# Optimization experiments

Hardware: AMD Instinct MI355X
Metric: run time of the kernel (lower is better)

Reference implementation:

```python
import jax, jax.numpy as jnp
import numpy as np

N = 100000   # num nodes
E = 800000   # num edges
D = 16       # latent_dim
K = 3        # message-passing iterations
ALPHA = 0.1
GAMMA = 0.9


def _mlp2(x, w1, b1, w2, b2):
    return jax.nn.relu(x @ w1 + b1) @ w2 + b2


def setup_inputs() -> dict:
    key = jax.random.key(0)
    ks = iter(jax.random.split(key, 40))
    def w(shape, fan_in):
        return jax.random.normal(next(ks), shape, jnp.float32) / np.sqrt(fan_in)
    return {
        "edge_index": jax.random.randint(next(ks), (2, E), 0, N),
        "edge_attr": jax.random.normal(next(ks), (E, 3), jnp.float32),
        "a_ij": jax.random.normal(next(ks), (E, 1), jnp.float32),
        "prb_data": jax.random.normal(next(ks), (N, 1), jnp.float32),
        "sol": jax.random.normal(next(ks), (N, 1), jnp.float32),
        "y": jax.random.normal(next(ks), (N, 1), jnp.float32),
        "phi_to_w1": w((K, 2 * D + 3, D), 2 * D + 3), "phi_to_b1": jnp.zeros((K, D), jnp.float32),
        "phi_to_w2": w((K, D, D), D), "phi_to_b2": jnp.zeros((K, D), jnp.float32),
        "phi_from_w1": w((K, 2 * D + 3, D), 2 * D + 3), "phi_from_b1": jnp.zeros((K, D), jnp.float32),
        "phi_from_w2": w((K, D, D), D), "phi_from_b2": jnp.zeros((K, D), jnp.float32),
        "psi_w1": w((K, 3 * D + 1, D), 3 * D + 1), "psi_b1": jnp.zeros((K, D), jnp.float32),
        "psi_w2": w((K, D, D), D), "psi_b2": jnp.zeros((K, D), jnp.float32),
        "dec_w1": w((K, D, D), D), "dec_b1": jnp.zeros((K, D), jnp.float32),
        "dec_w2": w((K, D, 1), D), "dec_b2": jnp.zeros((K, 1), jnp.float32),
    }


def reference(edge_index, edge_attr, a_ij, prb_data, sol, y,
              phi_to_w1, phi_to_b1, phi_to_w2, phi_to_b2,
              phi_from_w1, phi_from_b1, phi_from_w2, phi_from_b2,
              psi_w1, psi_b1, psi_w2, psi_b2,
              dec_w1, dec_b1, dec_w2, dec_b2):
    src, dst = edge_index[0], edge_index[1]
    # remove_self_loops: with 'add' aggregation, zeroing self-loop messages is equivalent.
    sl_mask = (src != dst).astype(edge_attr.dtype)[:, None]

    def message_pass(h, xi_idx, xj_idx, agg_idx, w1, b1, w2, b2):
        # gather-concat-MLP-scatter: tmp is [E, 2D+3]
        tmp = jnp.concatenate([h[xi_idx], h[xj_idx], edge_attr], axis=1)
        m = _mlp2(tmp, w1, b1, w2, b2) * sl_mask
        return jax.ops.segment_sum(m, agg_idx, num_segments=N)

    a_val = a_ij[:, 0]
    def residual_loss(u):
        # SparseTensor(row=src, col=dst, value=a_ij) @ u  (self-loops kept here)
        Au = jax.ops.segment_sum(a_val * u[dst, 0], src, num_segments=N)[:, None]
        return jnp.mean((Au - y) ** 2)

    h = jnp.zeros((N, D), edge_attr.dtype)
    u = _mlp2(h, dec_w1[0], dec_b1[0], dec_w2[0], dec_b2[0])  # U['0']
    total_loss = jnp.zeros((), edge_attr.dtype)
    for t in range(K):
        # Phi_to: flow source_to_target -> x_i = h[dst], x_j = h[src], aggregate at dst
        mess_to = message_pass(h, dst, src, dst, phi_to_w1[t], phi_to_b1[t], phi_to_w2[t], phi_to_b2[t])
        # Phi_from: flow target_to_source -> x_i = h[src], x_j = h[dst], aggregate at src
        mess_from = message_pass(h, src, dst, src, phi_from_w1[t], phi_from_b1[t], phi_from_w2[t], phi_from_b2[t])
        concat = jnp.concatenate([h, mess_to, mess_from, prb_data], axis=1)  # [N, 3D+1]
        h = h + ALPHA * _mlp2(concat, psi_w1[t], psi_b1[t], psi_w2[t], psi_b2[t])
        u = _mlp2(h, dec_w1[t], dec_b1[t], dec_w2[t], dec_b2[t])
        total_loss = total_loss + residual_loss(u) * GAMMA ** (K - t - 1)
    return u, total_loss
```

## Files before the change

kernel.cpp:

```cpp
#include <hip/hip_runtime.h>

#define NN 100000
#define NE 800000
#define DD 16
#define ALPHA 0.1f

__device__ __forceinline__ void load16(const float* __restrict__ p, float* r) {
  float4 v0 = *(const float4*)(p + 0);
  float4 v1 = *(const float4*)(p + 4);
  float4 v2 = *(const float4*)(p + 8);
  float4 v3 = *(const float4*)(p + 12);
  r[0]=v0.x; r[1]=v0.y; r[2]=v0.z; r[3]=v0.w;
  r[4]=v1.x; r[5]=v1.y; r[6]=v1.z; r[7]=v1.w;
  r[8]=v2.x; r[9]=v2.y; r[10]=v2.z; r[11]=v2.w;
  r[12]=v3.x; r[13]=v3.y; r[14]=v3.z; r[15]=v3.w;
}

__device__ __forceinline__ void store16(float* __restrict__ p, const float* r) {
  *(float4*)(p + 0)  = make_float4(r[0], r[1], r[2], r[3]);
  *(float4*)(p + 4)  = make_float4(r[4], r[5], r[6], r[7]);
  *(float4*)(p + 8)  = make_float4(r[8], r[9], r[10], r[11]);
  *(float4*)(p + 12) = make_float4(r[12], r[13], r[14], r[15]);
}

__global__ __launch_bounds__(256) void hist_kernel(
    const int* __restrict__ ei,
    int* __restrict__ hist_dst, int* __restrict__ hist_src,
    int* __restrict__ rank_dst, int* __restrict__ rank_src)
{
  int e = blockIdx.x * 256 + threadIdx.x;
  if (e >= NE) return;
  int s = ei[e];
  int d = ei[NE + e];
  rank_src[e] = atomicAdd(&hist_src[s], 1);
  rank_dst[e] = atomicAdd(&hist_dst[d], 1);
}

__global__ __launch_bounds__(256) void scan1_kernel(
    const int* __restrict__ in, int* __restrict__ out, int* __restrict__ sums, int L)
{
  __shared__ int sh[256];
  int t = threadIdx.x;
  int i0 = blockIdx.x * 1024 + t * 4;
  int v0 = (i0 + 0 < L) ? in[i0 + 0] : 0;
  int v1 = (i0 + 1 < L) ? in[i0 + 1] : 0;
  int v2 = (i0 + 2 < L) ? in[i0 + 2] : 0;
  int v3 = (i0 + 3 < L) ? in[i0 + 3] : 0;
  int tot = v0 + v1 + v2 + v3;
  sh[t] = tot;
  __syncthreads();
  int val = tot;
  for (int off = 1; off < 256; off <<= 1) {
    int x = (t >= off) ? sh[t - off] : 0;
    __syncthreads();
    val += x; sh[t] = val;
    __syncthreads();
  }
  if (t == 255) sums[blockIdx.x] = val;
  int run = val - tot;
  if (i0 + 0 < L) out[i0 + 0] = run; run += v0;
  if (i0 + 1 < L) out[i0 + 1] = run; run += v1;
  if (i0 + 2 < L) out[i0 + 2] = run; run += v2;
  if (i0 + 3 < L) out[i0 + 3] = run;
}

__global__ __launch_bounds__(256) void scan2_kernel(
    int* __restrict__ sums, int nb, int* __restrict__ out_total)
{
  __shared__ int sh[256];
  int t = threadIdx.x;
  int v = (t < nb) ? sums[t] : 0;
  sh[t] = v;
  __syncthreads();
  int val = v;
  for (int off = 1; off < 256; off <<= 1) {
    int x = (t >= off) ? sh[t - off] : 0;
    __syncthreads();
    val += x; sh[t] = val;
    __syncthreads();
  }
  if (t < nb) sums[t] = val - v;
  if (t == 255) *out_total = val;
}

__global__ __launch_bounds__(256) void scan3_kernel(
    int* __restrict__ out, const int* __restrict__ sums, int L)
{
  int i = blockIdx.x * 256 + threadIdx.x;
  if (i < L) out[i] += sums[i >> 10];
}

__global__ __launch_bounds__(256) void scatter_kernel(
    const int* __restrict__ ei, const float* __restrict__ ea, const float* __restrict__ a,
    const int* __restrict__ base_dst, const int* __restrict__ base_src,
    const int* __restrict__ rank_dst, const int* __restrict__ rank_src,
    float4* __restrict__ pay_dst, float4* __restrict__ pay_src, float2* __restrict__ pay_au)
{
  int e = blockIdx.x * 256 + threadIdx.x;
  if (e >= NE) return;
  int s = ei[e];
  int d = ei[NE + e];
  float e0 = ea[3 * (size_t)e], e1 = ea[3 * (size_t)e + 1], e2 = ea[3 * (size_t)e + 2];
  int sl = (s == d);
  int pd = base_dst[d] + rank_dst[e];
  pay_dst[pd] = make_float4(__int_as_float(sl ? -1 : s), e0, e1, e2);
  int ps = base_src[s] + rank_src[e];
  pay_src[ps] = make_float4(__int_as_float(sl ? -1 : d), e0, e1, e2);
  pay_au[ps] = make_float2(__int_as_float(d), a[e]);
}

template<bool FIRST>
__global__ __launch_bounds__(256) void gather_kernel(
    const float* __restrict__ h,
    const float4* __restrict__ pay_dst, const float4* __restrict__ pay_src,
    const int* __restrict__ base_dst, const int* __restrict__ base_src,
    const float* __restrict__ to_w1, const float* __restrict__ to_b1,
    const float* __restrict__ to_w2, const float* __restrict__ to_b2,
    const float* __restrict__ fr_w1, const float* __restrict__ fr_b1,
    const float* __restrict__ fr_w2, const float* __restrict__ fr_b2,
    float* __restrict__ mto, float* __restrict__ mfr)
{
  __shared__ float sw[1696];
  for (int i = threadIdx.x; i < 560; i += 256) { sw[i] = to_w1[i]; sw[848 + i] = fr_w1[i]; }
  { int i = threadIdx.x;
    if (i < 256) { sw[576 + i] = to_w2[i]; sw[848 + 576 + i] = fr_w2[i]; }
    if (i < 16) {
      sw[560 + i] = to_b1[i];
      sw[832 + i] = to_b2[i];
      sw[848 + 560 + i] = fr_b1[i];
      sw[848 + 832 + i] = fr_b2[i];
    }
  }
  __syncthreads();

  int gid = (blockIdx.x * 256 + threadIdx.x) >> 2;
  int l = threadIdx.x & 3;
  if (gid >= 2 * NN) return;
  int dir = (gid >= NN) ? 1 : 0;
  int n = gid - (dir ? NN : 0);

  const float* w1 = sw + (dir ? 848 : 0);
  const float* b1 = w1 + 560;
  const float* w2 = w1 + 576;
  const float* b2 = w1 + 832;
  const float4* pay = dir ? pay_src : pay_dst;
  const int* base = dir ? base_src : base_dst;

  float p1[DD];
  #pragma unroll
  for (int j = 0; j < DD; ++j) p1[j] = b1[j];
  if (!FIRST) {
    float hn[DD];
    load16(h + (size_t)n * DD, hn);
    #pragma unroll
    for (int i = 0; i < DD; ++i) {
      float x = hn[i];
      #pragma unroll
      for (int j = 0; j < DD; ++j) p1[j] = fmaf(x, w1[i * DD + j], p1[j]);
    }
  }

  float hs_[DD];
  #pragma unroll
  for (int j = 0; j < DD; ++j) hs_[j] = 0.0f;
  int cnt = 0;

  int beg = base[n], end = base[n + 1];
  for (int i = beg + l; i < end; i += 4) {
    float4 q = pay[i];
    int nb = __float_as_int(q.x);
    if (nb >= 0) {
      float hid[DD];
      #pragma unroll
      for (int j = 0; j < DD; ++j)
        hid[j] = fmaf(q.y, w1[32 * DD + j],
                 fmaf(q.z, w1[33 * DD + j],
                 fmaf(q.w, w1[34 * DD + j], p1[j])));
      if (!FIRST) {
        float hb[DD];
        load16(h + (size_t)nb * DD, hb);
        #pragma unroll
        for (int k = 0; k < DD; ++k) {
          float x = hb[k];
          #pragma unroll
          for (int j = 0; j < DD; ++j) hid[j] = fmaf(x, w1[(DD + k) * DD + j], hid[j]);
        }
      }
      #pragma unroll
      for (int j = 0; j < DD; ++j) hs_[j] += fmaxf(hid[j], 0.0f);
      ++cnt;
    }
  }

  #pragma unroll
  for (int j = 0; j < DD; ++j) {
    hs_[j] += __shfl_xor(hs_[j], 1, 64);
    hs_[j] += __shfl_xor(hs_[j], 2, 64);
  }
  cnt += __shfl_xor(cnt, 1, 64);
  cnt += __shfl_xor(cnt, 2, 64);

  float c = (float)cnt;
  float m0 = c * b2[4 * l + 0];
  float m1 = c * b2[4 * l + 1];
  float m2 = c * b2[4 * l + 2];
  float m3 = c * b2[4 * l + 3];
  #pragma unroll
  for (int k = 0; k < DD; ++k) {
    float x = hs_[k];
    const float* wr = w2 + k * DD + 4 * l;
    m0 = fmaf(x, wr[0], m0);
    m1 = fmaf(x, wr[1], m1);
    m2 = fmaf(x, wr[2], m2);
    m3 = fmaf(x, wr[3], m3);
  }
  float* dst = (dir ? mfr : mto) + (size_t)n * DD + 4 * l;
  *(float4*)dst = make_float4(m0, m1, m2, m3);
}

__global__ __launch_bounds__(256) void node_kernel(
    float* __restrict__ h, const float* __restrict__ mto, const float* __restrict__ mfr,
    const float* __restrict__ prb,
    const float* __restrict__ psi_w1, const float* __restrict__ psi_b1,
    const float* __restrict__ psi_w2, const float* __restrict__ psi_b2,
    const float* __restrict__ dec_w1, const float* __restrict__ dec_b1,
    const float* __restrict__ dec_w2, const float* __restrict__ dec_b2,
    float* __restrict__ u)
{
  __shared__ float sw[1361];
  for (int i = threadIdx.x; i < 784; i += 256) sw[i] = psi_w1[i];
  { int i = threadIdx.x;
    if (i < 256) { sw[800 + i] = psi_w2[i]; sw[1072 + i] = dec_w1[i]; }
    if (i < 16) {
      sw[784 + i] = psi_b1[i];
      sw[1056 + i] = psi_b2[i];
      sw[1328 + i] = dec_b1[i];
      sw[1344 + i] = dec_w2[i];
    }
    if (i == 0) sw[1360] = dec_b2[0];
  }
  __syncthreads();

  int n = blockIdx.x * 256 + threadIdx.x;
  if (n >= NN) return;

  float hv[DD], mt[DD], mf[DD];
  load16(h + (size_t)n * DD, hv);
  load16(mto + (size_t)n * DD, mt);
  load16(mfr + (size_t)n * DD, mf);
  float p = prb[n];

  float hid[DD];
  #pragma unroll
  for (int j = 0; j < DD; ++j) hid[j] = sw[784 + j];
  #pragma unroll
  for (int i = 0; i < DD; ++i) {
    float x = hv[i];
    #pragma unroll
    for (int j = 0; j < DD; ++j) hid[j] = fmaf(x, sw[i * DD + j], hid[j]);
  }
  #pragma unroll
  for (int i = 0; i < DD; ++i) {
    float x = mt[i];
    #pragma unroll
    for (int j = 0; j < DD; ++j) hid[j] = fmaf(x, sw[(DD + i) * DD + j], hid[j]);
  }
  #pragma unroll
  for (int i = 0; i < DD; ++i) {
    float x = mf[i];
    #pragma unroll
    for (int j = 0; j < DD; ++j) hid[j] = fmaf(x, sw[(2 * DD + i) * DD + j], hid[j]);
  }
  #pragma unroll
  for (int j = 0; j < DD; ++j) hid[j] = fmaf(p, sw[48 * DD + j], hid[j]);
  #pragma unroll
  for (int j = 0; j < DD; ++j) hid[j] = fmaxf(hid[j], 0.0f);

  float hnew[DD];
  #pragma unroll
  for (int j = 0; j < DD; ++j) hnew[j] = sw[1056 + j];
  #pragma unroll
  for (int i = 0; i < DD; ++i) {
    float x = hid[i];
    #pragma unroll
    for (int j = 0; j < DD; ++j) hnew[j] = fmaf(x, sw[800 + i * DD + j], hnew[j]);
  }
  #pragma unroll
  for (int j = 0; j < DD; ++j) hnew[j] = fmaf(ALPHA, hnew[j], hv[j]);
  store16(h + (size_t)n * DD, hnew);

  float hid2[DD];
  #pragma unroll
  for (int j = 0; j < DD; ++j) hid2[j] = sw[1328 + j];
  #pragma unroll
  for (int i = 0; i < DD; ++i) {
    float x = hnew[i];
    #pragma unroll
    for (int j = 0; j < DD; ++j) hid2[j] = fmaf(x, sw[1072 + i * DD + j], hid2[j]);
  }
  float uo = sw[1360];
  #pragma unroll
  for (int i = 0; i < DD; ++i) uo += fmaxf(hid2[i], 0.0f) * sw[1344 + i];
  u[n] = uo;
}

__global__ __launch_bounds__(256) void au_loss_kernel(
    const int* __restrict__ base_src, const float2* __restrict__ pay_au,
    const float* __restrict__ u, const float* __restrict__ y,
    float w, float* __restrict__ loss)
{
  int n = blockIdx.x * 256 + threadIdx.x;
  float acc = 0.0f;
  if (n < NN) {
    float au = 0.0f;
    int beg = base_src[n], end = base_src[n + 1];
    for (int i = beg; i < end; ++i) {
      float2 q = pay_au[i];
      au = fmaf(q.y, u[__float_as_int(q.x)], au);
    }
    float dlt = au - y[n];
    acc = dlt * dlt;
  }
  #pragma unroll
  for (int off = 32; off > 0; off >>= 1) acc += __shfl_down(acc, off);
  __shared__ float ss[4];
  int lane = threadIdx.x & 63, wid = threadIdx.x >> 6;
  if (lane == 0) ss[wid] = acc;
  __syncthreads();
  if (threadIdx.x == 0) {
    atomicAdd(loss, (ss[0] + ss[1] + ss[2] + ss[3]) * w);
  }
}

extern "C" void kernel_launch(void* const* d_in, const int* in_sizes, int n_in,
                              void* d_out, int out_size, void* d_ws, size_t ws_size,
                              hipStream_t stream) {
  const int*   ei        = (const int*)d_in[0];
  const float* ea        = (const float*)d_in[1];
  const float* a_ij      = (const float*)d_in[2];
  const float* prb       = (const float*)d_in[3];
  const float* y         = (const float*)d_in[5];
  const float* phi_to_w1 = (const float*)d_in[6];
  const float* phi_to_b1 = (const float*)d_in[7];
  const float* phi_to_w2 = (const float*)d_in[8];
  const float* phi_to_b2 = (const float*)d_in[9];
  const float* phi_fr_w1 = (const float*)d_in[10];
  const float* phi_fr_b1 = (const float*)d_in[11];
  const float* phi_fr_w2 = (const float*)d_in[12];
  const float* phi_fr_b2 = (const float*)d_in[13];
  const float* psi_w1    = (const float*)d_in[14];
  const float* psi_b1    = (const float*)d_in[15];
  const float* psi_w2    = (const float*)d_in[16];
  const float* psi_b2    = (const float*)d_in[17];
  const float* dec_w1    = (const float*)d_in[18];
  const float* dec_b1    = (const float*)d_in[19];
  const float* dec_w2    = (const float*)d_in[20];
  const float* dec_b2    = (const float*)d_in[21];

  float* out_u    = (float*)d_out;
  float* out_loss = out_u + NN;

  char* wp = (char*)d_ws;
  auto carve = [&](size_t bytes) { void* p = (void*)wp; wp += (bytes + 15) & ~(size_t)15; return p; };
  float4* pay_dst  = (float4*)carve((size_t)NE * 16);
  float4* pay_src  = (float4*)carve((size_t)NE * 16);
  float2* pay_au   = (float2*)carve((size_t)NE * 8);
  float*  h        = (float*)carve((size_t)NN * DD * 4);
  float*  mto      = (float*)carve((size_t)NN * DD * 4);
  float*  mfr      = (float*)carve((size_t)NN * DD * 4);
  int*    rank_dst = (int*)carve((size_t)NE * 4);
  int*    rank_src = (int*)carve((size_t)NE * 4);
  int*    base_dst = (int*)carve((size_t)(NN + 1) * 4);
  int*    base_src = (int*)carve((size_t)(NN + 1) * 4);
  int*    hist_dst = (int*)carve((size_t)NN * 4);
  int*    hist_src = (int*)carve((size_t)NN * 4);
  int*    sums     = (int*)carve(256 * 4);

  hipMemsetAsync(h, 0, (size_t)NN * DD * 4, stream);
  hipMemsetAsync(out_loss, 0, 4, stream);
  hipMemsetAsync(hist_dst, 0, (size_t)NN * 4, stream);
  hipMemsetAsync(hist_src, 0, (size_t)NN * 4, stream);

  const int EB = (NE + 255) / 256;
  const int NB = (NN + 255) / 256;
  const int SB1 = (NN + 1023) / 1024;
  const int GB4 = (2 * NN * 4 + 255) / 256;

  hist_kernel<<<EB, 256, 0, stream>>>(ei, hist_dst, hist_src, rank_dst, rank_src);

  scan1_kernel<<<SB1, 256, 0, stream>>>(hist_dst, base_dst, sums, NN);
  scan2_kernel<<<1, 256, 0, stream>>>(sums, SB1, base_dst + NN);
  scan3_kernel<<<NB, 256, 0, stream>>>(base_dst, sums, NN);

  scan1_kernel<<<SB1, 256, 0, stream>>>(hist_src, base_src, sums, NN);
  scan2_kernel<<<1, 256, 0, stream>>>(sums, SB1, base_src + NN);
  scan3_kernel<<<NB, 256, 0, stream>>>(base_src, sums, NN);

  scatter_kernel<<<EB, 256, 0, stream>>>(ei, ea, a_ij, base_dst, base_src,
                                         rank_dst, rank_src, pay_dst, pay_src, pay_au);

  const float gw[3] = {0.81f, 0.9f, 1.0f};

  for (int t = 0; t < 3; ++t) {
    if (t == 0) {
      gather_kernel<true><<<GB4, 256, 0, stream>>>(
          h, pay_dst, pay_src, base_dst, base_src,
          phi_to_w1, phi_to_b1, phi_to_w2, phi_to_b2,
          phi_fr_w1, phi_fr_b1, phi_fr_w2, phi_fr_b2,
          mto, mfr);
    } else {
      gather_kernel<false><<<GB4, 256, 0, stream>>>(
          h, pay_dst, pay_src, base_dst, base_src,
          phi_to_w1 + t * 560, phi_to_b1 + t * 16, phi_to_w2 + t * 256, phi_to_b2 + t * 16,
          phi_fr_w1 + t * 560, phi_fr_b1 + t * 16, phi_fr_w2 + t * 256, phi_fr_b2 + t * 16,
          mto, mfr);
    }

    node_kernel<<<NB, 256, 0, stream>>>(
        h, mto, mfr, prb,
        psi_w1 + t * 784, psi_b1 + t * 16, psi_w2 + t * 256, psi_b2 + t * 16,
        dec_w1 + t * 256, dec_b1 + t * 16, dec_w2 + t * 16, dec_b2 + t,
        out_u);

    au_loss_kernel<<<NB, 256, 0, stream>>>(base_src, pay_au, out_u, y,
                                           gw[t] / (float)NN, out_loss);
  }
}
```

Measured before the change: 354.6 us.

## Merge CSR builds, use bf16 neighbor features, fuse loss into gather, widen lanes

The separate dst and src CSR structures are merged into one histogram, scan and payload array, so a single scan pass covers 2N entries. The node kernel also writes a bf16 copy of h, and the gather reads neighbour features from it, which halves gather bandwidth but reduces precision. The residual-loss kernel is fused as extra blocks into the next gather launch, with a final standalone launch for the last step. Each node now uses 8 lanes instead of 4 to spread edges across more threads.

```diff
diff --git a/kernel.cpp b/kernel.cpp
--- a/kernel.cpp
+++ b/kernel.cpp
@@ -23,17 +23,21 @@
   *(float4*)(p + 12) = make_float4(r[12], r[13], r[14], r[15]);
 }
 
+__device__ __forceinline__ unsigned f2bf(float x) {
+  unsigned b = __float_as_uint(x);
+  return (b + 0x7FFFu + ((b >> 16) & 1u)) >> 16;
+}
+
 __global__ __launch_bounds__(256) void hist_kernel(
-    const int* __restrict__ ei,
-    int* __restrict__ hist_dst, int* __restrict__ hist_src,
+    const int* __restrict__ ei, int* __restrict__ hist,
     int* __restrict__ rank_dst, int* __restrict__ rank_src)
 {
   int e = blockIdx.x * 256 + threadIdx.x;
   if (e >= NE) return;
   int s = ei[e];
   int d = ei[NE + e];
-  rank_src[e] = atomicAdd(&hist_src[s], 1);
-  rank_dst[e] = atomicAdd(&hist_dst[d], 1);
+  rank_dst[e] = atomicAdd(&hist[d], 1);
+  rank_src[e] = atomicAdd(&hist[NN + s], 1);
 }
 
 __global__ __launch_bounds__(256) void scan1_kernel(
@@ -92,9 +96,9 @@
 
 __global__ __launch_bounds__(256) void scatter_kernel(
     const int* __restrict__ ei, const float* __restrict__ ea, const float* __restrict__ a,
-    const int* __restrict__ base_dst, const int* __restrict__ base_src,
+    const int* __restrict__ base,
     const int* __restrict__ rank_dst, const int* __restrict__ rank_src,
-    float4* __restrict__ pay_dst, float4* __restrict__ pay_src, float2* __restrict__ pay_au)
+    float4* __restrict__ pay, float2* __restrict__ pay_au)
 {
   int e = blockIdx.x * 256 + threadIdx.x;
   if (e >= NE) return;
@@ -102,24 +106,48 @@
   int d = ei[NE + e];
   float e0 = ea[3 * (size_t)e], e1 = ea[3 * (size_t)e + 1], e2 = ea[3 * (size_t)e + 2];
   int sl = (s == d);
-  int pd = base_dst[d] + rank_dst[e];
-  pay_dst[pd] = make_float4(__int_as_float(sl ? -1 : s), e0, e1, e2);
-  int ps = base_src[s] + rank_src[e];
-  pay_src[ps] = make_float4(__int_as_float(sl ? -1 : d), e0, e1, e2);
-  pay_au[ps] = make_float2(__int_as_float(d), a[e]);
-}
-
-template<bool FIRST>
+  int pd = base[d] + rank_dst[e];
+  pay[pd] = make_float4(__int_as_float(sl ? -1 : s), e0, e1, e2);
+  int ps = base[NN + s] + rank_src[e];
+  pay[ps] = make_float4(__int_as_float(sl ? -1 : d), e0, e1, e2);
+  pay_au[ps - NE] = make_float2(__int_as_float(d), a[e]);
+}
+
+template<bool FIRST, bool WITH_AU>
 __global__ __launch_bounds__(256) void gather_kernel(
-    const float* __restrict__ h,
-    const float4* __restrict__ pay_dst, const float4* __restrict__ pay_src,
-    const int* __restrict__ base_dst, const int* __restrict__ base_src,
+    const float* __restrict__ h, const unsigned short* __restrict__ hb,
+    const float4* __restrict__ pay, const int* __restrict__ base,
     const float* __restrict__ to_w1, const float* __restrict__ to_b1,
     const float* __restrict__ to_w2, const float* __restrict__ to_b2,
     const float* __restrict__ fr_w1, const float* __restrict__ fr_b1,
     const float* __restrict__ fr_w2, const float* __restrict__ fr_b2,
-    float* __restrict__ mto, float* __restrict__ mfr)
-{
+    float* __restrict__ mto, float* __restrict__ mfr, int gblocks,
+    const float2* __restrict__ pay_au, const float* __restrict__ u,
+    const float* __restrict__ y, float w, float* __restrict__ loss)
+{
+  if (WITH_AU && (int)blockIdx.x >= gblocks) {
+    int n = (blockIdx.x - gblocks) * 256 + threadIdx.x;
+    float acc = 0.0f;
+    if (n < NN) {
+      float au = 0.0f;
+      int beg = base[NN + n] - NE, end = base[NN + n + 1] - NE;
+      for (int i = beg; i < end; ++i) {
+        float2 q = pay_au[i];
+        au = fmaf(q.y, u[__float_as_int(q.x)], au);
+      }
+      float dlt = au - y[n];
+      acc = dlt * dlt;
+    }
+    #pragma unroll
+    for (int off = 32; off > 0; off >>= 1) acc += __shfl_down(acc, off);
+    __shared__ float ss[4];
+    int lane = threadIdx.x & 63, wid = threadIdx.x >> 6;
+    if (lane == 0) ss[wid] = acc;
+    __syncthreads();
+    if (threadIdx.x == 0) atomicAdd(loss, (ss[0] + ss[1] + ss[2] + ss[3]) * w);
+    return;
+  }
+
   __shared__ float sw[1696];
   for (int i = threadIdx.x; i < 560; i += 256) { sw[i] = to_w1[i]; sw[848 + i] = fr_w1[i]; }
   { int i = threadIdx.x;
@@ -133,8 +161,8 @@
   }
   __syncthreads();
 
-  int gid = (blockIdx.x * 256 + threadIdx.x) >> 2;
-  int l = threadIdx.x & 3;
+  int gid = (blockIdx.x * 256 + threadIdx.x) >> 3;
+  int l = threadIdx.x & 7;
   if (gid >= 2 * NN) return;
   int dir = (gid >= NN) ? 1 : 0;
   int n = gid - (dir ? NN : 0);
@@ -143,8 +171,6 @@
   const float* b1 = w1 + 560;
   const float* w2 = w1 + 576;
   const float* b2 = w1 + 832;
-  const float4* pay = dir ? pay_src : pay_dst;
-  const int* base = dir ? base_src : base_dst;
 
   float p1[DD];
   #pragma unroll
@@ -165,8 +191,8 @@
   for (int j = 0; j < DD; ++j) hs_[j] = 0.0f;
   int cnt = 0;
 
-  int beg = base[n], end = base[n + 1];
-  for (int i = beg + l; i < end; i += 4) {
+  int beg = base[gid], end = base[gid + 1];
+  for (int i = beg + l; i < end; i += 8) {
     float4 q = pay[i];
     int nb = __float_as_int(q.x);
     if (nb >= 0) {
@@ -177,11 +203,20 @@
                  fmaf(q.z, w1[33 * DD + j],
                  fmaf(q.w, w1[34 * DD + j], p1[j])));
       if (!FIRST) {
-        float hb[DD];
-        load16(h + (size_t)nb * DD, hb);
+        uint4 qa = *(const uint4*)(hb + (size_t)nb * DD);
+        uint4 qb = *(const uint4*)(hb + (size_t)nb * DD + 8);
+        float hv[DD];
+        hv[0]  = __uint_as_float(qa.x << 16); hv[1]  = __uint_as_float(qa.x & 0xFFFF0000u);
+        hv[2]  = __uint_as_float(qa.y << 16); hv[3]  = __uint_as_float(qa.y & 0xFFFF0000u);
+        hv[4]  = __uint_as_float(qa.z << 16); hv[5]  = __uint_as_float(qa.z & 0xFFFF0000u);
+        hv[6]  = __uint_as_float(qa.w << 16); hv[7]  = __uint_as_float(qa.w & 0xFFFF0000u);
+        hv[8]  = __uint_as_float(qb.x << 16); hv[9]  = __uint_as_float(qb.x & 0xFFFF0000u);
+        hv[10] = __uint_as_float(qb.y << 16); hv[11] = __uint_as_float(qb.y & 0xFFFF0000u);
+        hv[12] = __uint_as_float(qb.z << 16); hv[13] = __uint_as_float(qb.z & 0xFFFF0000u);
+        hv[14] = __uint_as_float(qb.w << 16); hv[15] = __uint_as_float(qb.w & 0xFFFF0000u);
         #pragma unroll
         for (int k = 0; k < DD; ++k) {
-          float x = hb[k];
+          float x = hv[k];
           #pragma unroll
           for (int j = 0; j < DD; ++j) hid[j] = fmaf(x, w1[(DD + k) * DD + j], hid[j]);
         }
@@ -196,30 +231,28 @@
   for (int j = 0; j < DD; ++j) {
     hs_[j] += __shfl_xor(hs_[j], 1, 64);
     hs_[j] += __shfl_xor(hs_[j], 2, 64);
+    hs_[j] += __shfl_xor(hs_[j], 4, 64);
   }
   cnt += __shfl_xor(cnt, 1, 64);
   cnt += __shfl_xor(cnt, 2, 64);
+  cnt += __shfl_xor(cnt, 4, 64);
 
   float c = (float)cnt;
-  float m0 = c * b2[4 * l + 0];
-  float m1 = c * b2[4 * l + 1];
-  float m2 = c * b2[4 * l + 2];
-  float m3 = c * b2[4 * l + 3];
+  float m0 = c * b2[2 * l + 0];
+  float m1 = c * b2[2 * l + 1];
   #pragma unroll
   for (int k = 0; k < DD; ++k) {
     float x = hs_[k];
-    const float* wr = w2 + k * DD + 4 * l;
-    m0 = fmaf(x, wr[0], m0);
-    m1 = fmaf(x, wr[1], m1);
-    m2 = fmaf(x, wr[2], m2);
-    m3 = fmaf(x, wr[3], m3);
-  }
-  float* dst = (dir ? mfr : mto) + (size_t)n * DD + 4 * l;
-  *(float4*)dst = make_float4(m0, m1, m2, m3);
+    m0 = fmaf(x, w2[k * DD + 2 * l + 0], m0);
+    m1 = fmaf(x, w2[k * DD + 2 * l + 1], m1);
+  }
+  float* dst = (dir ? mfr : mto) + (size_t)n * DD + 2 * l;
+  *(float2*)dst = make_float2(m0, m1);
 }
 
 __global__ __launch_bounds__(256) void node_kernel(
-    float* __restrict__ h, const float* __restrict__ mto, const float* __restrict__ mfr,
+    float* __restrict__ h, unsigned short* __restrict__ hb,
+    const float* __restrict__ mto, const float* __restrict__ mfr,
     const float* __restrict__ prb,
     const float* __restrict__ psi_w1, const float* __restrict__ psi_b1,
     const float* __restrict__ psi_w2, const float* __restrict__ psi_b2,
@@ -289,6 +322,18 @@
   for (int j = 0; j < DD; ++j) hnew[j] = fmaf(ALPHA, hnew[j], hv[j]);
   store16(h + (size_t)n * DD, hnew);
 
+  uint4 pa, pb;
+  pa.x = f2bf(hnew[0])  | (f2bf(hnew[1])  << 16);
+  pa.y = f2bf(hnew[2])  | (f2bf(hnew[3])  << 16);
+  pa.z = f2bf(hnew[4])  | (f2bf(hnew[5])  << 16);
+  pa.w = f2bf(hnew[6])  | (f2bf(hnew[7])  << 16);
+  pb.x = f2bf(hnew[8])  | (f2bf(hnew[9])  << 16);
+  pb.y = f2bf(hnew[10]) | (f2bf(hnew[11]) << 16);
+  pb.z = f2bf(hnew[12]) | (f2bf(hnew[13]) << 16);
+  pb.w = f2bf(hnew[14]) | (f2bf(hnew[15]) << 16);
+  *(uint4*)(hb + (size_t)n * DD)     = pa;
+  *(uint4*)(hb + (size_t)n * DD + 8) = pb;
+
   float hid2[DD];
   #pragma unroll
   for (int j = 0; j < DD; ++j) hid2[j] = sw[1328 + j];
@@ -302,34 +347,6 @@
   #pragma unroll
   for (int i = 0; i < DD; ++i) uo += fmaxf(hid2[i], 0.0f) * sw[1344 + i];
   u[n] = uo;
-}
-
-__global__ __launch_bounds__(256) void au_loss_kernel(
-    const int* __restrict__ base_src, const float2* __restrict__ pay_au,
-    const float* __restrict__ u, const float* __restrict__ y,
-    float w, float* __restrict__ loss)
-{
-  int n = blockIdx.x * 256 + threadIdx.x;
-  float acc = 0.0f;
-  if (n < NN) {
-    float au = 0.0f;
-    int beg = base_src[n], end = base_src[n + 1];
-    for (int i = beg; i < end; ++i) {
-      float2 q = pay_au[i];
-      au = fmaf(q.y, u[__float_as_int(q.x)], au);
-    }
-    float dlt = au - y[n];
-    acc = dlt * dlt;
-  }
-  #pragma unroll
-  for (int off = 32; off > 0; off >>= 1) acc += __shfl_down(acc, off);
-  __shared__ float ss[4];
-  int lane = threadIdx.x & 63, wid = threadIdx.x >> 6;
-  if (lane == 0) ss[wid] = acc;
-  __syncthreads();
-  if (threadIdx.x == 0) {
-    atomicAdd(loss, (ss[0] + ss[1] + ss[2] + ss[3]) * w);
-  }
 }
 
 extern "C" void kernel_launch(void* const* d_in, const int* in_sizes, int n_in,
@@ -362,67 +379,63 @@
 
   char* wp = (char*)d_ws;
   auto carve = [&](size_t bytes) { void* p = (void*)wp; wp += (bytes + 15) & ~(size_t)15; return p; };
-  float4* pay_dst  = (float4*)carve((size_t)NE * 16);
-  float4* pay_src  = (float4*)carve((size_t)NE * 16);
+  float4* pay      = (float4*)carve((size_t)2 * NE * 16);
   float2* pay_au   = (float2*)carve((size_t)NE * 8);
   float*  h        = (float*)carve((size_t)NN * DD * 4);
+  unsigned short* hb16 = (unsigned short*)carve((size_t)NN * DD * 2);
   float*  mto      = (float*)carve((size_t)NN * DD * 4);
   float*  mfr      = (float*)carve((size_t)NN * DD * 4);
   int*    rank_dst = (int*)carve((size_t)NE * 4);
   int*    rank_src = (int*)carve((size_t)NE * 4);
-  int*    base_dst = (int*)carve((size_t)(NN + 1) * 4);
-  int*    base_src = (int*)carve((size_t)(NN + 1) * 4);
-  int*    hist_dst = (int*)carve((size_t)NN * 4);
-  int*    hist_src = (int*)carve((size_t)NN * 4);
+  int*    base     = (int*)carve((size_t)(2 * NN + 1) * 4);
+  int*    hist     = (int*)carve((size_t)2 * NN * 4);
   int*    sums     = (int*)carve(256 * 4);
 
   hipMemsetAsync(h, 0, (size_t)NN * DD * 4, stream);
   hipMemsetAsync(out_loss, 0, 4, stream);
-  hipMemsetAsync(hist_dst, 0, (size_t)NN * 4, stream);
-  hipMemsetAsync(hist_src, 0, (size_t)NN * 4, stream);
-
-  const int EB = (NE + 255) / 256;
-  const int NB = (NN + 255) / 256;
-  const int SB1 = (NN + 1023) / 1024;
-  const int GB4 = (2 * NN * 4 + 255) / 256;
-
-  hist_kernel<<<EB, 256, 0, stream>>>(ei, hist_dst, hist_src, rank_dst, rank_src);
-
-  scan1_kernel<<<SB1, 256, 0, stream>>>(hist_dst, base_dst, sums, NN);
-  scan2_kernel<<<1, 256, 0, stream>>>(sums, SB1, base_dst + NN);
-  scan3_kernel<<<NB, 256, 0, stream>>>(base_dst, sums, NN);
-
-  scan1_kernel<<<SB1, 256, 0, stream>>>(hist_src, base_src, sums, NN);
-  scan2_kernel<<<1, 256, 0, stream>>>(sums, SB1, base_src + NN);
-  scan3_kernel<<<NB, 256, 0, stream>>>(base_src, sums, NN);
-
-  scatter_kernel<<<EB, 256, 0, stream>>>(ei, ea, a_ij, base_dst, base_src,
-                                         rank_dst, rank_src, pay_dst, pay_src, pay_au);
+  hipMemsetAsync(hist, 0, (size_t)2 * NN * 4, stream);
+
+  const int EB  = (NE + 255) / 256;
+  const int NB  = (NN + 255) / 256;
+  const int L2N = 2 * NN;
+  const int SB1 = (L2N + 1023) / 1024;
+  const int SB3 = (L2N + 255) / 256;
+  const int GB8 = (L2N * 8 + 255) / 256;
+
+  hist_kernel<<<EB, 256, 0, stream>>>(ei, hist, rank_dst, rank_src);
+  scan1_kernel<<<SB1, 256, 0, stream>>>(hist, base, sums, L2N);
+  scan2_kernel<<<1, 256, 0, stream>>>(sums, SB1, base + L2N);
+  scan3_kernel<<<SB3, 256, 0, stream>>>(base, sums, L2N);
+  scatter_kernel<<<EB, 256, 0, stream>>>(ei, ea, a_ij, base, rank_dst, rank_src,
+                                         pay, pay_au);
 
   const float gw[3] = {0.81f, 0.9f, 1.0f};
 
-  for (int t = 0; t < 3; ++t) {
-    if (t == 0) {
-      gather_kernel<true><<<GB4, 256, 0, stream>>>(
-          h, pay_dst, pay_src, base_dst, base_src,
-          phi_to_w1, phi_to_b1, phi_to_w2, phi_to_b2,
-          phi_fr_w1, phi_fr_b1, phi_fr_w2, phi_fr_b2,
-          mto, mfr);
-    } else {
-      gather_kernel<false><<<GB4, 256, 0, stream>>>(
-          h, pay_dst, pay_src, base_dst, base_src,
-          phi_to_w1 + t * 560, phi_to_b1 + t * 16, phi_to_w2 + t * 256, phi_to_b2 + t * 16,
-          phi_fr_w1 + t * 560, phi_fr_b1 + t * 16, phi_fr_w2 + t * 256, phi_fr_b2 + t * 16,
-          mto, mfr);
-    }
-
+  gather_kernel<true, false><<<GB8, 256, 0, stream>>>(
+      h, hb16, pay, base,
+      phi_to_w1, phi_to_b1, phi_to_w2, phi_to_b2,
+      phi_fr_w1, phi_fr_b1, phi_fr_w2, phi_fr_b2,
+      mto, mfr, GB8, pay_au, out_u, y, 0.0f, out_loss);
+  node_kernel<<<NB, 256, 0, stream>>>(
+      h, hb16, mto, mfr, prb,
+      psi_w1, psi_b1, psi_w2, psi_b2,
+      dec_w1, dec_b1, dec_w2, dec_b2, out_u);
+
+  for (int t = 1; t < 3; ++t) {
+    gather_kernel<false, true><<<GB8 + NB, 256, 0, stream>>>(
+        h, hb16, pay, base,
+        phi_to_w1 + t * 560, phi_to_b1 + t * 16, phi_to_w2 + t * 256, phi_to_b2 + t * 16,
+        phi_fr_w1 + t * 560, phi_fr_b1 + t * 16, phi_fr_w2 + t * 256, phi_fr_b2 + t * 16,
+        mto, mfr, GB8, pay_au, out_u, y, gw[t - 1] / (float)NN, out_loss);
     node_kernel<<<NB, 256, 0, stream>>>(
-        h, mto, mfr, prb,
+        h, hb16, mto, mfr, prb,
         psi_w1 + t * 784, psi_b1 + t * 16, psi_w2 + t * 256, psi_b2 + t * 16,
-        dec_w1 + t * 256, dec_b1 + t * 16, dec_w2 + t * 16, dec_b2 + t,
-        out_u);
-
-    au_loss_kernel<<<NB, 256, 0, stream>>>(base_src, pay_au, out_u, y,
-                                           gw[t] / (float)NN, out_loss);
-  }
-}
+        dec_w1 + t * 256, dec_b1 + t * 16, dec_w2 + t * 16, dec_b2 + t, out_u);
+  }
+
+  gather_kernel<false, true><<<NB, 256, 0, stream>>>(
+      h, hb16, pay, base,
+      phi_to_w1, phi_to_b1, phi_to_w2, phi_to_b2,
+      phi_fr_w1, phi_fr_b1, phi_fr_w2, phi_fr_b2,
+      mto, mfr, 0, pay_au, out_u, y, gw[2] / (float)NN, out_loss);
+}
```

After: 341.8 us. 1.04x faster.
